# Kernel optimization log

Hardware: AMD Instinct MI355X
Metric: run time of the kernel (lower is better)

## Reference

```python
import jax, jax.numpy as jnp
import numpy as np

B, F, C, H, W = 16, 256, 64, 64, 64   # batch, features, z_channels(e_dim), height, width
N_E = 512                              # codebooksize
BETA = 1.0
EPS = 1e-5


def setup_inputs() -> dict:
    key = jax.random.key(0)
    ks = jax.random.split(key, 4)
    x = jax.random.normal(ks[0], (B, F, H, W), jnp.float32)
    emb = jax.random.normal(ks[1], (N_E, C), jnp.float32)
    emb = emb / jnp.linalg.norm(emb, axis=1, keepdims=True)  # points on hypersphere
    return dict(
        x=x,
        bn1_gamma=jnp.ones((F,), jnp.float32),
        bn1_beta=jnp.zeros((F,), jnp.float32),
        conv1_w=jax.random.normal(ks[2], (C, F), jnp.float32) * np.float32(1.0 / np.sqrt(F)),
        conv1_b=jnp.zeros((C,), jnp.float32),
        conv2_w=jax.random.normal(ks[3], (C, C), jnp.float32) * np.float32(1.0 / np.sqrt(C)),
        conv2_b=jnp.zeros((C,), jnp.float32),
        embedding=emb,
        r=jnp.ones((N_E,), jnp.float32),
    )


def reference(x, bn1_gamma, bn1_beta, conv1_w, conv1_b, conv2_w, conv2_b, embedding, r):
    sg = jax.lax.stop_gradient
    # BatchNorm2d (training mode: batch stats, biased variance)
    mu = x.mean(axis=(0, 2, 3), keepdims=True)
    var = x.var(axis=(0, 2, 3), keepdims=True)
    x1 = (x - mu) * jax.lax.rsqrt(var + EPS)
    x1 = x1 * bn1_gamma[None, :, None, None] + bn1_beta[None, :, None, None]
    # 1x1 convs (note: original overwrites norm2 output, conv2 consumes conv1 output directly)
    x1 = jnp.einsum('bfhw,cf->bchw', x1, conv1_w) + conv1_b[None, :, None, None]
    z = jnp.einsum('bchw,oc->bohw', x1, conv2_w) + conv2_b[None, :, None, None]

    zf = z.reshape(-1, C)  # [B*C*H*W/e_dim view == flat rows of e_dim]
    # codebook angular statistics (norms detached, as torch.Tensor(list) detaches)
    d1 = embedding @ embedding.T                                 # [n_e, n_e]
    en = sg(jnp.linalg.norm(embedding, axis=1))                  # [n_e]
    edx = jnp.clip(d1 / (en[:, None] * en[None, :]), -0.99999, 0.99999)
    ang = jnp.arccos(edx)
    total_min_distance = jnp.mean(jnp.sort(ang, axis=0)[1])      # kthvalue(.,2,dim=0)
    codebookvariance = jnp.mean(jnp.var(ang, axis=1, ddof=1))    # torch.var unbiased

    # VQ dispatch: squared L2 distances + argmin + gather
    d = (zf ** 2).sum(1, keepdims=True) + (embedding ** 2).sum(1) - 2.0 * (zf @ embedding.T)
    idx = jnp.argmin(d, axis=1)                                  # [ntok]
    z_q = embedding[idx].reshape(z.shape)

    hsw = jnp.mean(jnp.square(r - en))
    # legacy=True path with beta=1.0, ignorezq=False, disentangle=True
    loss = jnp.mean((sg(z_q) - z) ** 2) + BETA * jnp.mean((z_q - sg(z)) ** 2)
    loss = loss + hsw + (codebookvariance - total_min_distance)

    z_q = z + sg(z_q - z)  # straight-through
    cb_loss = jnp.float32(0.0)  # prev_cb is None
    r_c = r + sg(jnp.clip(r, 0.9, 1.1) - r)  # Clamp with straight-through grad
    mean_r = jnp.mean(r_c)
    return (loss, z_q, codebookvariance, total_min_distance, hsw, cb_loss, mean_r)
```

## Files before the change

### kernel.cpp

```cpp
#include <hip/hip_runtime.h>
#include <math.h>


#define CAP    2048
#define MARGIN 4e-3f

#define WS_WHI  0
#define WS_WLO  8192
#define WS_BP   16384
#define WS_EN   16448
#define WS_E2   16960
#define WS_ACC  17472
#define WS_CNT  17480
#define WS_WL   17488
#define WS_EFT  19536
#define WS_WD   52304
#define WS_BPD  85072
#define WS_PART 85200
#define WS_EHI  87248
#define WS_ELO  103632

typedef __attribute__((ext_vector_type(8))) __bf16 bf16v8;
typedef __attribute__((ext_vector_type(2))) __bf16 bf16v2;
typedef __attribute__((ext_vector_type(4))) float  f32v4;
typedef __attribute__((ext_vector_type(4))) unsigned u32v4;

__device__ __forceinline__ unsigned short f2bf(float f) {
    __bf16 h = (__bf16)f;
    return __builtin_bit_cast(unsigned short, h);
}
__device__ __forceinline__ float bf2f(unsigned short h) {
    union { unsigned u; float f; } v; v.u = ((unsigned)h) << 16; return v.f;
}
__device__ __forceinline__ unsigned pack_bf2(float a, float b) {
    bf16v2 v = { (__bf16)a, (__bf16)b };
    return __builtin_bit_cast(unsigned, v);
}
__device__ __forceinline__ float bfhi(float a) {
    return (float)(__bf16)a;
}
__device__ __forceinline__ void load_lds16(const float* g, unsigned* l) {
    __builtin_amdgcn_global_load_lds((const __attribute__((address_space(1))) void*)g,
                                     (__attribute__((address_space(3))) void*)l, 16, 0, 0);
}

__global__ __launch_bounds__(256) void bn_partial(
    const float* __restrict__ x, double* __restrict__ part)
{
    const int f = blockIdx.x >> 1, ch = blockIdx.x & 1, t = threadIdx.x;
    double s = 0.0, q = 0.0;
    #pragma unroll 1
    for (int bb = 0; bb < 8; ++bb) {
        const int b = ch * 8 + bb;
        const float4* p = (const float4*)(x + ((size_t)(b * 256 + f) << 12));
        #pragma unroll
        for (int ii = 0; ii < 4; ++ii) {
            float4 u = p[t + ii * 256];
            double dx = u.x, dy = u.y, dz = u.z, dw = u.w;
            s += (dx + dy) + (dz + dw);
            q = fma(dx, dx, q); q = fma(dy, dy, q);
            q = fma(dz, dz, q); q = fma(dw, dw, q);
        }
    }
    #pragma unroll
    for (int off = 32; off; off >>= 1) { s += __shfl_xor(s, off, 64); q += __shfl_xor(q, off, 64); }
    __shared__ double sh[8];
    const int wv = t >> 6;
    if ((t & 63) == 0) { sh[wv * 2] = s; sh[wv * 2 + 1] = q; }
    __syncthreads();
    if (t == 0) {
        part[blockIdx.x * 2]     = (sh[0] + sh[2]) + (sh[4] + sh[6]);
        part[blockIdx.x * 2 + 1] = (sh[1] + sh[3]) + (sh[5] + sh[7]);
    }
}

__global__ __launch_bounds__(256) void prep(
    const float* __restrict__ w1, const float* __restrict__ w2,
    const float* __restrict__ b1, const float* __restrict__ b2,
    const float* __restrict__ gamma, const float* __restrict__ beta,
    const float* __restrict__ emb, const double* __restrict__ part,
    unsigned short* __restrict__ whi, unsigned short* __restrict__ wlo,
    double* __restrict__ Wd,
    double* __restrict__ bpd, float* __restrict__ bp,
    float* __restrict__ eft, float* __restrict__ en, float* __restrict__ e2,
    unsigned short* __restrict__ ehi, unsigned short* __restrict__ elo,
    float* __restrict__ accs, int* __restrict__ cnt)
{
    __shared__ double sh_ad[4];
    __shared__ double cdl[256];
    __shared__ double red[4][64];
    __shared__ double tsh[64];
    const int t = threadIdx.x;

    if (blockIdx.x < 64) {
        const int o = t & 63, fi = t >> 6;
        const int f = blockIdx.x * 4 + fi;
        if (o == 0) {
            double s = part[(2 * f) * 2]     + part[(2 * f + 1) * 2];
            double q = part[(2 * f) * 2 + 1] + part[(2 * f + 1) * 2 + 1];
            double mean = s * (1.0 / 65536.0);
            double var  = q * (1.0 / 65536.0) - mean * mean;
            sh_ad[fi] = (double)gamma[f] / sqrt(var + 1e-5);
        }
        __syncthreads();
        double s = 0.0;
        for (int c = 0; c < 64; ++c)
            s = fma((double)w2[o * 64 + c], (double)w1[c * 256 + f], s);
        double wp = s * sh_ad[fi];
        Wd[o * 256 + f] = wp;
        {
            float wpf = (float)wp;
            unsigned short wh = f2bf(wpf);
            unsigned short wlv = f2bf(wpf - bf2f(wh));
            int mt = o >> 4, cq_ = o & 15, sK = f >> 5, qd_ = (f >> 3) & 3, j = f & 7;
            int idx = ((mt * 8 + sK) * 64 + qd_ * 16 + cq_) * 8 + j;
            whi[idx] = wh; wlo[idx] = wlv;
        }

        const int lane = t & 63, wv = t >> 6;
        #pragma unroll
        for (int rr = 0; rr < 2; ++rr) {
            int n = blockIdx.x * 8 + rr * 4 + wv;
            float v = emb[n * 64 + lane];
            eft[lane * 512 + n] = v;
            unsigned short hb = f2bf(v);
            unsigned short lb = f2bf(v - bf2f(hb));
            int pos = (lane >> 3) ^ (n & 7);
            ehi[n * 64 + pos * 8 + (lane & 7)] = hb;
            elo[n * 64 + pos * 8 + (lane & 7)] = lb;
            float qq = v * v;
            #pragma unroll
            for (int off = 32; off; off >>= 1) qq += __shfl_xor(qq, off, 64);
            if (lane == 0) { e2[n] = qq; en[n] = sqrtf(qq); }
        }
    } else {
        {
            const int f = t;
            double s = part[(2 * f) * 2]     + part[(2 * f + 1) * 2];
            double q = part[(2 * f) * 2 + 1] + part[(2 * f + 1) * 2 + 1];
            double mean = s * (1.0 / 65536.0);
            double var  = q * (1.0 / 65536.0) - mean * mean;
            double a = (double)gamma[f] / sqrt(var + 1e-5);
            cdl[f] = (double)beta[f] - mean * a;
        }
        __syncthreads();
        const int o = t & 63, p = t >> 6;
        double ss = 0.0;
        for (int j = 0; j < 64; ++j) {
            int fidx = p * 64 + j;
            ss = fma((double)w1[o * 256 + fidx], cdl[fidx], ss);
        }
        red[p][o] = ss; __syncthreads();
        if (t < 64) tsh[t] = (double)b1[t] + (red[0][t] + red[1][t]) + (red[2][t] + red[3][t]);
        __syncthreads();
        if (t < 64) {
            double bb = (double)b2[t];
            for (int c = 0; c < 64; ++c)
                bb = fma((double)w2[t * 64 + c], tsh[c], bb);
            bpd[t] = bb;
            bp[t]  = (float)bb;
        }
        if (t < 8) accs[t] = 0.f;
        if (t == 0) cnt[0] = 0;
    }
}

__global__ __launch_bounds__(256, 2) void fused_gemm_vq(
    const float* __restrict__ x,
    const unsigned short* __restrict__ whi,
    const unsigned short* __restrict__ wlo,
    const float* __restrict__ bp,
    const float* __restrict__ emb,
    const float* __restrict__ e2,
    const float* __restrict__ en,
    const float* __restrict__ eft,
    const unsigned short* __restrict__ ehi,
    const unsigned short* __restrict__ elo,
    float* __restrict__ accs,
    int* __restrict__ cnt, int* __restrict__ wl,
    float* __restrict__ zq)
{
    __shared__ __align__(16) unsigned smem[4880];
    enum { OAR = 0,
           OE2 = 4096, OZ2 = 4608, ODT = 4672, OD2T = 4736, OIT = 4800 };
    float* e2s = (float*)(smem + OE2);
    float* z2s = (float*)(smem + OZ2);
    float* dT  = (float*)(smem + ODT);
    float* d2T = (float*)(smem + OD2T);
    int*   iT  = (int*)(smem + OIT);

    const int tid = threadIdx.x, lane = tid & 63, wv = tid >> 6;

    if (blockIdx.x >= 1024) {
        const int i = blockIdx.x - 1024;
        float* ang = e2s;
        const float eni = en[i];
        const float* ei = emb + (i << 6);
        #pragma unroll
        for (int jj = 0; jj < 2; ++jj) {
            const int j = tid + jj * 256;
            float d0 = 0.f, d1 = 0.f, d2 = 0.f, d3 = 0.f;
            #pragma unroll
            for (int k = 0; k < 64; k += 4) {
                d0 = fmaf(ei[k + 0], eft[(k + 0) * 512 + j], d0);
                d1 = fmaf(ei[k + 1], eft[(k + 1) * 512 + j], d1);
                d2 = fmaf(ei[k + 2], eft[(k + 2) * 512 + j], d2);
                d3 = fmaf(ei[k + 3], eft[(k + 3) * 512 + j], d3);
            }
            float dot = (d0 + d1) + (d2 + d3);
            float xv = dot / (eni * en[j]);
            xv = fminf(fmaxf(xv, -0.99999f), 0.99999f);
            ang[j] = acosf(xv);
        }
        __syncthreads();
        if (wv == 0) {
            float m1 = 3.4e38f, m2 = 3.4e38f, ssum = 0.f;
            #pragma unroll
            for (int t8 = 0; t8 < 8; ++t8) {
                float a = ang[t8 * 64 + lane];
                ssum += a;
                if (a < m1) { m2 = m1; m1 = a; }
                else if (a < m2) m2 = a;
            }
            #pragma unroll
            for (int off = 32; off; off >>= 1) ssum += __shfl_xor(ssum, off, 64);
            #pragma unroll
            for (int off = 32; off; off >>= 1) {
                float o1 = __shfl_xor(m1, off, 64);
                float o2 = __shfl_xor(m2, off, 64);
                if (o1 < m1) { m2 = fminf(m1, o2); m1 = o1; }
                else          m2 = fminf(m2, o1);
            }
            float mean = ssum * (1.f / 512.f);
            float vs = 0.f;
            #pragma unroll
            for (int t8 = 0; t8 < 8; ++t8) {
                float tt = ang[t8 * 64 + lane] - mean;
                vs = fmaf(tt, tt, vs);
            }
            #pragma unroll
            for (int off = 32; off; off >>= 1) vs += __shfl_xor(vs, off, 64);
            if (lane == 0) {
                atomicAdd(accs + 1, vs * (1.f / 511.f));
                atomicAdd(accs + 2, m2);
            }
        }
        return;
    }

    const int wvu = __builtin_amdgcn_readfirstlane(wv);
    const int b = blockIdx.x >> 6, h = blockIdx.x & 63;
    const int cq = lane & 15, qd = lane >> 4;

    bf16v8 Ahi[8], Alo[8];
    #pragma unroll
    for (int s = 0; s < 8; ++s) {
        Ahi[s] = *(const bf16v8*)(whi + ((size_t)((wvu * 8 + s) * 64 + lane)) * 8);
        Alo[s] = *(const bf16v8*)(wlo + ((size_t)((wvu * 8 + s) * 64 + lane)) * 8);
    }
    float bpv[4];
    #pragma unroll
    for (int r = 0; r < 4; ++r) bpv[r] = bp[wvu * 16 + qd * 4 + r];
    e2s[tid]       = e2[tid];
    e2s[tid + 256] = e2[tid + 256];

    const float* xb = x + ((size_t)(b * 256 + wvu * 16) << 12) + (h << 6) + lane;
    float xv[16];
    #pragma unroll
    for (int i = 0; i < 16; ++i) xv[i] = xb[(size_t)i << 12];

    f32v4 acc[4];
    #pragma unroll
    for (int nt = 0; nt < 4; ++nt) acc[nt] = (f32v4){bpv[0], bpv[1], bpv[2], bpv[3]};

    #pragma unroll
    for (int chk = 0; chk < 4; ++chk) {
        __syncthreads();
        {
            unsigned hb[8], lb[8];
            #pragma unroll
            for (int p = 0; p < 8; ++p) {
                float a = xv[2 * p], bq = xv[2 * p + 1];
                hb[p] = pack_bf2(a, bq);
                lb[p] = pack_bf2(a - bfhi(a), bq - bfhi(bq));
            }
            const int b0 = lane * 32 + (((2 * wvu) ^ (lane & 7)) << 2);
            const int b1 = lane * 32 + (((2 * wvu + 1) ^ (lane & 7)) << 2);
            *(u32v4*)(smem + OAR + b0)        = (u32v4){hb[0], hb[1], hb[2], hb[3]};
            *(u32v4*)(smem + OAR + b1)        = (u32v4){hb[4], hb[5], hb[6], hb[7]};
            *(u32v4*)(smem + OAR + 2048 + b0) = (u32v4){lb[0], lb[1], lb[2], lb[3]};
            *(u32v4*)(smem + OAR + 2048 + b1) = (u32v4){lb[4], lb[5], lb[6], lb[7]};
        }
        __syncthreads();
        if (chk < 3) {
            const float* xb2 = xb + ((size_t)((chk + 1) * 64) << 12);
            #pragma unroll
            for (int i = 0; i < 16; ++i) xv[i] = xb2[(size_t)i << 12];
        }
        #pragma unroll
        for (int st2 = 0; st2 < 2; ++st2) {
            const int s = chk * 2 + st2;
            #pragma unroll
            for (int nt = 0; nt < 4; ++nt) {
                const int row = nt * 16 + cq;
                const int pos = row * 32 + (((st2 * 4 + qd) ^ (row & 7)) << 2);
                bf16v8 bh = *(const bf16v8*)(smem + OAR + pos);
                bf16v8 bl = *(const bf16v8*)(smem + OAR + 2048 + pos);
                acc[nt] = __builtin_amdgcn_mfma_f32_16x16x32_bf16(Ahi[s], bh, acc[nt], 0, 0, 0);
                acc[nt] = __builtin_amdgcn_mfma_f32_16x16x32_bf16(Ahi[s], bl, acc[nt], 0, 0, 0);
                acc[nt] = __builtin_amdgcn_mfma_f32_16x16x32_bf16(Alo[s], bh, acc[nt], 0, 0, 0);
            }
        }
    }
    __syncthreads();

    {
        float z2p[4];
        #pragma unroll
        for (int r = 0; r < 4; ++r) {
            float p2 = 0.f;
            #pragma unroll
            for (int nt = 0; nt < 4; ++nt) p2 = fmaf(acc[nt][r], acc[nt][r], p2);
            #pragma unroll
            for (int off = 1; off <= 8; off <<= 1) p2 += __shfl_xor(p2, off, 64);
            z2p[r] = p2;
        }
        if (cq == 0) {
            #pragma unroll
            for (int r = 0; r < 4; ++r) z2s[wvu * 16 + qd * 4 + r] = z2p[r];
        }
        unsigned short* ar = (unsigned short*)(smem + OAR);
        #pragma unroll
        for (int nt = 0; nt < 4; ++nt) {
            const int w = nt * 16 + cq;
            const int gz = w >> 3, kj = w & 7;
            #pragma unroll
            for (int r = 0; r < 4; ++r) {
                const int tok = wvu * 16 + qd * 4 + r;
                const int hw = tok * 64 + ((gz ^ (tok & 7)) << 3) + kj;
                unsigned short zh = f2bf(acc[nt][r]);
                ar[hw]        = zh;
                ar[4096 + hw] = f2bf(acc[nt][r] - bf2f(zh));
            }
        }
    }
    __syncthreads();

    const int x7 = cq & 7;
    bf16v8 vahi[2], valo[2];
    {
        const int rbase = (wvu * 16 + cq) * 32;
        #pragma unroll
        for (int s = 0; s < 2; ++s) {
            int pos = ((s * 4 + qd) ^ x7) * 4;
            vahi[s] = *(const bf16v8*)(smem + OAR + rbase + pos);
            valo[s] = *(const bf16v8*)(smem + OAR + 2048 + rbase + pos);
        }
    }
    __syncthreads();

    {
        const float* gh = (const float*)ehi;
        const float* gl = (const float*)elo;
        load_lds16(gh + wvu * 256 + lane * 4,        smem + OAR + wvu * 256);
        load_lds16(gl + wvu * 256 + lane * 4,        smem + OAR + 1024 + wvu * 256);
        load_lds16(gh + 1024 + wvu * 256 + lane * 4, smem + OAR + 2048 + wvu * 256);
        load_lds16(gl + 1024 + wvu * 256 + lane * 4, smem + OAR + 3072 + wvu * 256);
    }

    float m1[4] = {-3.4e38f, -3.4e38f, -3.4e38f, -3.4e38f};
    float m2[4] = {-3.4e38f, -3.4e38f, -3.4e38f, -3.4e38f};
    int   i1[4] = {0, 0, 0, 0};
    const int p0 = (qd ^ x7) * 4, p1 = ((4 + qd) ^ x7) * 4;

    #pragma unroll 1
    for (int t2 = 0; t2 < 32; ++t2) {
        if ((t2 & 1) == 0) {
            __syncthreads();
            int st = t2 >> 1;
            if (st >= 1 && st < 15) {
                const float* gh = (const float*)ehi + (size_t)(st + 1) * 1024;
                const float* gl = (const float*)elo + (size_t)(st + 1) * 1024;
                unsigned* dst = smem + OAR + ((st + 1) & 1) * 2048;
                load_lds16(gh + wvu * 256 + lane * 4, dst + wvu * 256);
                load_lds16(gl + wvu * 256 + lane * 4, dst + 1024 + wvu * 256);
            }
        }
        const int rb = OAR + ((t2 >> 1) & 1) * 2048 + ((t2 & 1) * 16 + cq) * 32;
        bf16v8 bh0 = *(const bf16v8*)(smem + rb + p0);
        bf16v8 bh1 = *(const bf16v8*)(smem + rb + p1);
        bf16v8 bl0 = *(const bf16v8*)(smem + rb + 1024 + p0);
        bf16v8 bl1 = *(const bf16v8*)(smem + rb + 1024 + p1);
        const float eps = e2s[t2 * 16 + cq];
        f32v4 a = {0.f, 0.f, 0.f, 0.f};
        __builtin_amdgcn_s_setprio(1);
        a = __builtin_amdgcn_mfma_f32_16x16x32_bf16(vahi[0], bh0, a, 0, 0, 0);
        a = __builtin_amdgcn_mfma_f32_16x16x32_bf16(vahi[1], bh1, a, 0, 0, 0);
        a = __builtin_amdgcn_mfma_f32_16x16x32_bf16(vahi[0], bl0, a, 0, 0, 0);
        a = __builtin_amdgcn_mfma_f32_16x16x32_bf16(vahi[1], bl1, a, 0, 0, 0);
        a = __builtin_amdgcn_mfma_f32_16x16x32_bf16(valo[0], bh0, a, 0, 0, 0);
        a = __builtin_amdgcn_mfma_f32_16x16x32_bf16(valo[1], bh1, a, 0, 0, 0);
        __builtin_amdgcn_s_setprio(0);
        const int n = t2 * 16 + cq;
        #pragma unroll
        for (int r = 0; r < 4; ++r) {
            float s = fmaf(-0.5f, eps, a[r]);
            bool gt = s > m1[r];
            m2[r] = fminf(fmaxf(s, m2[r]), m1[r]);
            i1[r] = gt ? n : i1[r];
            m1[r] = fmaxf(s, m1[r]);
        }
    }

    #pragma unroll
    for (int r = 0; r < 4; ++r) {
        #pragma unroll
        for (int off = 1; off <= 8; off <<= 1) {
            float o1 = __shfl_xor(m1[r], off, 64);
            float o2 = __shfl_xor(m2[r], off, 64);
            int   oi = __shfl_xor(i1[r], off, 64);
            if (o1 > m1[r] || (o1 == m1[r] && oi < i1[r])) {
                m2[r] = fmaxf(m1[r], o2); m1[r] = o1; i1[r] = oi;
            } else {
                m2[r] = fmaxf(m2[r], o1);
            }
        }
    }
    if (cq == 0) {
        #pragma unroll
        for (int r = 0; r < 4; ++r) {
            int tok = wvu * 16 + qd * 4 + r;
            dT[tok] = m1[r]; d2T[tok] = m2[r]; iT[tok] = i1[r];
        }
    }
    __syncthreads();

    if (wv == 0) {
        float s1 = dT[lane], s2 = d2T[lane];
        if (s1 - s2 < MARGIN * 0.5f) {
            int pos = atomicAdd(cnt, 1);
            if (pos < CAP) wl[pos] = ((b << 6) + lane) * 64 + h;
        }
        float ms = z2s[lane] - 2.f * s1;
        #pragma unroll
        for (int off = 32; off; off >>= 1) ms += __shfl_xor(ms, off, 64);
        if (lane == 0) atomicAdd(accs + 0, ms);
    }
    __syncthreads();

    float* zrow = zq + ((size_t)(b * 64) << 12) + (h << 6) + lane;
    #pragma unroll
    for (int cc = 0; cc < 16; ++cc) {
        int c = wvu * 16 + cc;
        int id = iT[c];
        zrow[(size_t)c << 12] = emb[(id << 6) + lane];
    }
}

__global__ __launch_bounds__(256) void refine_fin(
    const float* __restrict__ x,
    const double* __restrict__ Wd,
    const double* __restrict__ bpd,
    const float* __restrict__ emb,
    const float* __restrict__ eft,
    const int* __restrict__ cnt, const int* __restrict__ wl,
    float* __restrict__ zq,
    const float* __restrict__ accs, const float* __restrict__ en,
    const float* __restrict__ r, float* __restrict__ out)
{
    const int tid = threadIdx.x, lane = tid & 63, wv = tid >> 6;

    if (blockIdx.x == 256) {
        if (wv == 0) {
            float hs = 0.f, rs = 0.f;
            #pragma unroll
            for (int jj = 0; jj < 8; ++jj) {
                int n = (jj << 6) + lane;
                float rv = r[n];
                float d = rv - en[n];
                hs = fmaf(d, d, hs);
                rs += fminf(fmaxf(rv, 0.9f), 1.1f);
            }
            #pragma unroll
            for (int off = 32; off; off >>= 1) { hs += __shfl_xor(hs, off, 64); rs += __shfl_xor(rs, off, 64); }
            if (lane == 0) {
                float hsw    = hs * (1.f / 512.f);
                float mean_r = rs * (1.f / 512.f);
                float mse    = accs[0] * (1.f / 4194304.f);
                float cbv    = accs[1] * (1.f / 512.f);
                float tmd    = accs[2] * (1.f / 512.f);
                float loss   = 2.f * mse + hsw + (cbv - tmd);
                out[0]       = loss;
                out[4194305] = cbv;
                out[4194306] = tmd;
                out[4194307] = hsw;
                out[4194308] = 0.f;
                out[4194309] = mean_r;
            }
        }
        return;
    }

    int count = cnt[0]; if (count > CAP) count = CAP;

    __shared__ double zp[4][64];
    __shared__ double zs[64];
    __shared__ double dsh[256];
    __shared__ int    ish[256];

    for (int it = blockIdx.x; it < count; it += 256) {
        const int r2 = wl[it];
        const int b = r2 >> 12, c = (r2 >> 6) & 63, h = r2 & 63;

        const float* xp = x + (((size_t)(b * 256 + wv * 64)) << 12) + (h << 6) + lane;
        const double* wrow = Wd + c * 256 + wv * 64;
        double z0 = 0.0, z1 = 0.0, z2a = 0.0, z3 = 0.0;
        #pragma unroll
        for (int f = 0; f < 64; f += 4) {
            float a0 = xp[(size_t)(f + 0) << 12];
            float a1 = xp[(size_t)(f + 1) << 12];
            float a2 = xp[(size_t)(f + 2) << 12];
            float a3 = xp[(size_t)(f + 3) << 12];
            z0  = fma(wrow[f + 0], (double)a0, z0);
            z1  = fma(wrow[f + 1], (double)a1, z1);
            z2a = fma(wrow[f + 2], (double)a2, z2a);
            z3  = fma(wrow[f + 3], (double)a3, z3);
        }
        zp[wv][lane] = (z0 + z1) + (z2a + z3);
        __syncthreads();
        if (tid < 64) zs[tid] = (zp[0][tid] + zp[1][tid]) + (zp[2][tid] + zp[3][tid]) + bpd[c];
        __syncthreads();

        double dm = 1e300; int im = 0;
        #pragma unroll
        for (int jj = 0; jj < 2; ++jj) {
            int n = (jj << 8) + tid;
            double da = 0.0, db = 0.0;
            #pragma unroll 8
            for (int k = 0; k < 64; k += 2) {
                double t0 = zs[k]     - (double)eft[(k << 9) + n];
                double t1 = zs[k + 1] - (double)eft[((k + 1) << 9) + n];
                da = fma(t0, t0, da); db = fma(t1, t1, db);
            }
            double d = da + db;
            if (d < dm) { dm = d; im = n; }
        }
        dsh[tid] = dm; ish[tid] = im;
        __syncthreads();
        for (int st = 128; st; st >>= 1) {
            if (tid < st) {
                double od = dsh[tid + st]; int oi = ish[tid + st];
                if (od < dsh[tid] || (od == dsh[tid] && oi < ish[tid])) { dsh[tid] = od; ish[tid] = oi; }
            }
            __syncthreads();
        }
        if (tid < 64) {
            int idx = ish[0];
            zq[((size_t)r2 << 6) + tid] = emb[(idx << 6) + tid];
        }
        __syncthreads();
    }
}

extern "C" void kernel_launch(void* const* d_in, const int* in_sizes, int n_in,
                              void* d_out, int out_size, void* d_ws, size_t ws_size,
                              hipStream_t stream) {
    const float* x   = (const float*)d_in[0];
    const float* g1  = (const float*)d_in[1];
    const float* be1 = (const float*)d_in[2];
    const float* w1  = (const float*)d_in[3];
    const float* b1  = (const float*)d_in[4];
    const float* w2  = (const float*)d_in[5];
    const float* b2  = (const float*)d_in[6];
    const float* emb = (const float*)d_in[7];
    const float* r   = (const float*)d_in[8];
    float* ws = (float*)d_ws;
    float* out = (float*)d_out;

    double* WD   = (double*)(ws + WS_WD);
    double* BPD  = (double*)(ws + WS_BPD);
    double* PART = (double*)(ws + WS_PART);
    int*    CNT  = (int*)(ws + WS_CNT);
    int*    WL   = (int*)(ws + WS_WL);
    unsigned short* WHI = (unsigned short*)(ws + WS_WHI);
    unsigned short* WLO = (unsigned short*)(ws + WS_WLO);
    unsigned short* EHI = (unsigned short*)(ws + WS_EHI);
    unsigned short* ELO = (unsigned short*)(ws + WS_ELO);

    bn_partial<<<512, 256, 0, stream>>>(x, PART);
    prep<<<65, 256, 0, stream>>>(w1, w2, b1, b2, g1, be1, emb, PART,
                                 WHI, WLO, WD, BPD, ws + WS_BP,
                                 ws + WS_EFT, ws + WS_EN, ws + WS_E2,
                                 EHI, ELO, ws + WS_ACC, CNT);
    fused_gemm_vq<<<1536, 256, 0, stream>>>(x, WHI, WLO, ws + WS_BP,
                                            emb, ws + WS_E2, ws + WS_EN, ws + WS_EFT,
                                            EHI, ELO, ws + WS_ACC, CNT, WL, out + 1);
    refine_fin<<<257, 256, 0, stream>>>(x, WD, BPD, emb, ws + WS_EFT, CNT, WL,
                                        out + 1, ws + WS_ACC, ws + WS_EN, r, out);
}
```

Before: 185.9 us.

## Move codebook angle stats into BN stats kernel and split BN reduction finer

The 512 codebook-angle blocks move out of the fused GEMM/VQ kernel into the BN statistics kernel, computing norms directly from the embedding so they no longer depend on prep. This lets them overlap with the memory-bound BN pass and shrinks the GEMM grid to 1024 blocks. The BN partials are now split four ways per feature instead of two, giving more parallelism. Accumulator zeroing moves to a memset. The MFMA chain is also split into two independent accumulators and the refine distance loop gets four partial sums for more ILP. The codebook-stats blocks are recomputed from raw embeddings, which costs some extra arithmetic.

```diff
diff --git a/kernel.cpp b/kernel.cpp
--- a/kernel.cpp
+++ b/kernel.cpp
@@ -16,9 +16,9 @@
 #define WS_EFT  19536
 #define WS_WD   52304
 #define WS_BPD  85072
-#define WS_PART 85200
-#define WS_EHI  87248
-#define WS_ELO  103632
+#define WS_EHI  85200
+#define WS_ELO  101584
+#define WS_PART 117968
 
 typedef __attribute__((ext_vector_type(8))) __bf16 bf16v8;
 typedef __attribute__((ext_vector_type(2))) __bf16 bf16v2;
@@ -44,33 +44,109 @@
                                      (__attribute__((address_space(3))) void*)l, 16, 0, 0);
 }
 
-__global__ __launch_bounds__(256) void bn_partial(
-    const float* __restrict__ x, double* __restrict__ part)
+__global__ __launch_bounds__(256) void bn_stats(
+    const float* __restrict__ x, double* __restrict__ part,
+    const float* __restrict__ emb, float* __restrict__ accs)
 {
-    const int f = blockIdx.x >> 1, ch = blockIdx.x & 1, t = threadIdx.x;
-    double s = 0.0, q = 0.0;
-    #pragma unroll 1
-    for (int bb = 0; bb < 8; ++bb) {
-        const int b = ch * 8 + bb;
-        const float4* p = (const float4*)(x + ((size_t)(b * 256 + f) << 12));
-        #pragma unroll
-        for (int ii = 0; ii < 4; ++ii) {
-            float4 u = p[t + ii * 256];
-            double dx = u.x, dy = u.y, dz = u.z, dw = u.w;
-            s += (dx + dy) + (dz + dw);
-            q = fma(dx, dx, q); q = fma(dy, dy, q);
-            q = fma(dz, dz, q); q = fma(dw, dw, q);
-        }
-    }
-    #pragma unroll
-    for (int off = 32; off; off >>= 1) { s += __shfl_xor(s, off, 64); q += __shfl_xor(q, off, 64); }
-    __shared__ double sh[8];
-    const int wv = t >> 6;
-    if ((t & 63) == 0) { sh[wv * 2] = s; sh[wv * 2 + 1] = q; }
-    __syncthreads();
-    if (t == 0) {
-        part[blockIdx.x * 2]     = (sh[0] + sh[2]) + (sh[4] + sh[6]);
-        part[blockIdx.x * 2 + 1] = (sh[1] + sh[3]) + (sh[5] + sh[7]);
+    const int t = threadIdx.x;
+
+    if (blockIdx.x < 1024) {
+        const int f = blockIdx.x >> 2, ch = blockIdx.x & 3;
+        double s0 = 0.0, s1 = 0.0, q0 = 0.0, q1 = 0.0, q2 = 0.0, q3 = 0.0;
+        #pragma unroll
+        for (int bb = 0; bb < 4; ++bb) {
+            const int b = ch * 4 + bb;
+            const float4* p = (const float4*)(x + ((size_t)(b * 256 + f) << 12));
+            #pragma unroll
+            for (int ii = 0; ii < 4; ++ii) {
+                float4 u = p[t + ii * 256];
+                double dx = u.x, dy = u.y, dz = u.z, dw = u.w;
+                s0 += dx + dy; s1 += dz + dw;
+                q0 = fma(dx, dx, q0); q1 = fma(dy, dy, q1);
+                q2 = fma(dz, dz, q2); q3 = fma(dw, dw, q3);
+            }
+        }
+        double s = s0 + s1, q = (q0 + q1) + (q2 + q3);
+        #pragma unroll
+        for (int off = 32; off; off >>= 1) { s += __shfl_xor(s, off, 64); q += __shfl_xor(q, off, 64); }
+        __shared__ double sh[8];
+        const int wv = t >> 6;
+        if ((t & 63) == 0) { sh[wv * 2] = s; sh[wv * 2 + 1] = q; }
+        __syncthreads();
+        if (t == 0) {
+            part[blockIdx.x * 2]     = (sh[0] + sh[2]) + (sh[4] + sh[6]);
+            part[blockIdx.x * 2 + 1] = (sh[1] + sh[3]) + (sh[5] + sh[7]);
+        }
+    } else {
+        const int i = blockIdx.x - 1024;
+        const int lane = t & 63, wv = t >> 6;
+        __shared__ float ei_sh[64];
+        __shared__ float ang[512];
+        if (t < 64) ei_sh[t] = emb[(i << 6) + t];
+        __syncthreads();
+        float ni0 = 0.f, ni1 = 0.f, ni2 = 0.f, ni3 = 0.f;
+        #pragma unroll
+        for (int k = 0; k < 64; k += 4) {
+            ni0 = fmaf(ei_sh[k + 0], ei_sh[k + 0], ni0);
+            ni1 = fmaf(ei_sh[k + 1], ei_sh[k + 1], ni1);
+            ni2 = fmaf(ei_sh[k + 2], ei_sh[k + 2], ni2);
+            ni3 = fmaf(ei_sh[k + 3], ei_sh[k + 3], ni3);
+        }
+        const float eni = sqrtf((ni0 + ni1) + (ni2 + ni3));
+        #pragma unroll
+        for (int jj = 0; jj < 2; ++jj) {
+            const int j = t + jj * 256;
+            const float4* er = (const float4*)(emb + ((size_t)j << 6));
+            float d0 = 0.f, d1 = 0.f, d2 = 0.f, d3 = 0.f;
+            float n0 = 0.f, n1 = 0.f, n2 = 0.f, n3 = 0.f;
+            #pragma unroll
+            for (int k4 = 0; k4 < 16; ++k4) {
+                float4 u = er[k4];
+                const float* e4 = ei_sh + k4 * 4;
+                d0 = fmaf(u.x, e4[0], d0); d1 = fmaf(u.y, e4[1], d1);
+                d2 = fmaf(u.z, e4[2], d2); d3 = fmaf(u.w, e4[3], d3);
+                n0 = fmaf(u.x, u.x, n0);   n1 = fmaf(u.y, u.y, n1);
+                n2 = fmaf(u.z, u.z, n2);   n3 = fmaf(u.w, u.w, n3);
+            }
+            float dot = (d0 + d1) + (d2 + d3);
+            float enj = sqrtf((n0 + n1) + (n2 + n3));
+            float xv = dot / (eni * enj);
+            xv = fminf(fmaxf(xv, -0.99999f), 0.99999f);
+            ang[j] = acosf(xv);
+        }
+        __syncthreads();
+        if (wv == 0) {
+            float m1 = 3.4e38f, m2 = 3.4e38f, ssum = 0.f;
+            #pragma unroll
+            for (int t8 = 0; t8 < 8; ++t8) {
+                float a = ang[t8 * 64 + lane];
+                ssum += a;
+                if (a < m1) { m2 = m1; m1 = a; }
+                else if (a < m2) m2 = a;
+            }
+            #pragma unroll
+            for (int off = 32; off; off >>= 1) ssum += __shfl_xor(ssum, off, 64);
+            #pragma unroll
+            for (int off = 32; off; off >>= 1) {
+                float o1 = __shfl_xor(m1, off, 64);
+                float o2 = __shfl_xor(m2, off, 64);
+                if (o1 < m1) { m2 = fminf(m1, o2); m1 = o1; }
+                else          m2 = fminf(m2, o1);
+            }
+            float mean = ssum * (1.f / 512.f);
+            float vs = 0.f;
+            #pragma unroll
+            for (int t8 = 0; t8 < 8; ++t8) {
+                float tt = ang[t8 * 64 + lane] - mean;
+                vs = fmaf(tt, tt, vs);
+            }
+            #pragma unroll
+            for (int off = 32; off; off >>= 1) vs += __shfl_xor(vs, off, 64);
+            if (lane == 0) {
+                atomicAdd(accs + 1, vs * (1.f / 511.f));
+                atomicAdd(accs + 2, m2);
+            }
+        }
     }
 }
 
@@ -83,8 +159,7 @@
     double* __restrict__ Wd,
     double* __restrict__ bpd, float* __restrict__ bp,
     float* __restrict__ eft, float* __restrict__ en, float* __restrict__ e2,
-    unsigned short* __restrict__ ehi, unsigned short* __restrict__ elo,
-    float* __restrict__ accs, int* __restrict__ cnt)
+    unsigned short* __restrict__ ehi, unsigned short* __restrict__ elo)
 {
     __shared__ double sh_ad[4];
     __shared__ double cdl[256];
@@ -96,8 +171,10 @@
         const int o = t & 63, fi = t >> 6;
         const int f = blockIdx.x * 4 + fi;
         if (o == 0) {
-            double s = part[(2 * f) * 2]     + part[(2 * f + 1) * 2];
-            double q = part[(2 * f) * 2 + 1] + part[(2 * f + 1) * 2 + 1];
+            double s = (part[(4 * f) * 2]     + part[(4 * f + 1) * 2])
+                     + (part[(4 * f + 2) * 2] + part[(4 * f + 3) * 2]);
+            double q = (part[(4 * f) * 2 + 1]     + part[(4 * f + 1) * 2 + 1])
+                     + (part[(4 * f + 2) * 2 + 1] + part[(4 * f + 3) * 2 + 1]);
             double mean = s * (1.0 / 65536.0);
             double var  = q * (1.0 / 65536.0) - mean * mean;
             sh_ad[fi] = (double)gamma[f] / sqrt(var + 1e-5);
@@ -136,8 +213,10 @@
     } else {
         {
             const int f = t;
-            double s = part[(2 * f) * 2]     + part[(2 * f + 1) * 2];
-            double q = part[(2 * f) * 2 + 1] + part[(2 * f + 1) * 2 + 1];
+            double s = (part[(4 * f) * 2]     + part[(4 * f + 1) * 2])
+                     + (part[(4 * f + 2) * 2] + part[(4 * f + 3) * 2]);
+            double q = (part[(4 * f) * 2 + 1]     + part[(4 * f + 1) * 2 + 1])
+                     + (part[(4 * f + 2) * 2 + 1] + part[(4 * f + 3) * 2 + 1]);
             double mean = s * (1.0 / 65536.0);
             double var  = q * (1.0 / 65536.0) - mean * mean;
             double a = (double)gamma[f] / sqrt(var + 1e-5);
@@ -160,8 +239,6 @@
             bpd[t] = bb;
             bp[t]  = (float)bb;
         }
-        if (t < 8) accs[t] = 0.f;
-        if (t == 0) cnt[0] = 0;
     }
 }
 
@@ -172,8 +249,6 @@
     const float* __restrict__ bp,
     const float* __restrict__ emb,
     const float* __restrict__ e2,
-    const float* __restrict__ en,
-    const float* __restrict__ eft,
     const unsigned short* __restrict__ ehi,
     const unsigned short* __restrict__ elo,
     float* __restrict__ accs,
@@ -190,64 +265,6 @@
     int*   iT  = (int*)(smem + OIT);
 
     const int tid = threadIdx.x, lane = tid & 63, wv = tid >> 6;
-
-    if (blockIdx.x >= 1024) {
-        const int i = blockIdx.x - 1024;
-        float* ang = e2s;
-        const float eni = en[i];
-        const float* ei = emb + (i << 6);
-        #pragma unroll
-        for (int jj = 0; jj < 2; ++jj) {
-            const int j = tid + jj * 256;
-            float d0 = 0.f, d1 = 0.f, d2 = 0.f, d3 = 0.f;
-            #pragma unroll
-            for (int k = 0; k < 64; k += 4) {
-                d0 = fmaf(ei[k + 0], eft[(k + 0) * 512 + j], d0);
-                d1 = fmaf(ei[k + 1], eft[(k + 1) * 512 + j], d1);
-                d2 = fmaf(ei[k + 2], eft[(k + 2) * 512 + j], d2);
-                d3 = fmaf(ei[k + 3], eft[(k + 3) * 512 + j], d3);
-            }
-            float dot = (d0 + d1) + (d2 + d3);
-            float xv = dot / (eni * en[j]);
-            xv = fminf(fmaxf(xv, -0.99999f), 0.99999f);
-            ang[j] = acosf(xv);
-        }
-        __syncthreads();
-        if (wv == 0) {
-            float m1 = 3.4e38f, m2 = 3.4e38f, ssum = 0.f;
-            #pragma unroll
-            for (int t8 = 0; t8 < 8; ++t8) {
-                float a = ang[t8 * 64 + lane];
-                ssum += a;
-                if (a < m1) { m2 = m1; m1 = a; }
-                else if (a < m2) m2 = a;
-            }
-            #pragma unroll
-            for (int off = 32; off; off >>= 1) ssum += __shfl_xor(ssum, off, 64);
-            #pragma unroll
-            for (int off = 32; off; off >>= 1) {
-                float o1 = __shfl_xor(m1, off, 64);
-                float o2 = __shfl_xor(m2, off, 64);
-                if (o1 < m1) { m2 = fminf(m1, o2); m1 = o1; }
-                else          m2 = fminf(m2, o1);
-            }
-            float mean = ssum * (1.f / 512.f);
-            float vs = 0.f;
-            #pragma unroll
-            for (int t8 = 0; t8 < 8; ++t8) {
-                float tt = ang[t8 * 64 + lane] - mean;
-                vs = fmaf(tt, tt, vs);
-            }
-            #pragma unroll
-            for (int off = 32; off; off >>= 1) vs += __shfl_xor(vs, off, 64);
-            if (lane == 0) {
-                atomicAdd(accs + 1, vs * (1.f / 511.f));
-                atomicAdd(accs + 2, m2);
-            }
-        }
-        return;
-    }
-
     const int wvu = __builtin_amdgcn_readfirstlane(wv);
     const int b = blockIdx.x >> 6, h = blockIdx.x & 63;
     const int cq = lane & 15, qd = lane >> 4;
@@ -392,19 +409,19 @@
         bf16v8 bl0 = *(const bf16v8*)(smem + rb + 1024 + p0);
         bf16v8 bl1 = *(const bf16v8*)(smem + rb + 1024 + p1);
         const float eps = e2s[t2 * 16 + cq];
-        f32v4 a = {0.f, 0.f, 0.f, 0.f};
+        f32v4 a0 = {0.f, 0.f, 0.f, 0.f}, a1 = {0.f, 0.f, 0.f, 0.f};
         __builtin_amdgcn_s_setprio(1);
-        a = __builtin_amdgcn_mfma_f32_16x16x32_bf16(vahi[0], bh0, a, 0, 0, 0);
-        a = __builtin_amdgcn_mfma_f32_16x16x32_bf16(vahi[1], bh1, a, 0, 0, 0);
-        a = __builtin_amdgcn_mfma_f32_16x16x32_bf16(vahi[0], bl0, a, 0, 0, 0);
-        a = __builtin_amdgcn_mfma_f32_16x16x32_bf16(vahi[1], bl1, a, 0, 0, 0);
-        a = __builtin_amdgcn_mfma_f32_16x16x32_bf16(valo[0], bh0, a, 0, 0, 0);
-        a = __builtin_amdgcn_mfma_f32_16x16x32_bf16(valo[1], bh1, a, 0, 0, 0);
+        a0 = __builtin_amdgcn_mfma_f32_16x16x32_bf16(vahi[0], bh0, a0, 0, 0, 0);
+        a1 = __builtin_amdgcn_mfma_f32_16x16x32_bf16(vahi[1], bh1, a1, 0, 0, 0);
+        a0 = __builtin_amdgcn_mfma_f32_16x16x32_bf16(vahi[0], bl0, a0, 0, 0, 0);
+        a1 = __builtin_amdgcn_mfma_f32_16x16x32_bf16(vahi[1], bl1, a1, 0, 0, 0);
+        a0 = __builtin_amdgcn_mfma_f32_16x16x32_bf16(valo[0], bh0, a0, 0, 0, 0);
+        a1 = __builtin_amdgcn_mfma_f32_16x16x32_bf16(valo[1], bh1, a1, 0, 0, 0);
         __builtin_amdgcn_s_setprio(0);
         const int n = t2 * 16 + cq;
         #pragma unroll
         for (int r = 0; r < 4; ++r) {
-            float s = fmaf(-0.5f, eps, a[r]);
+            float s = fmaf(-0.5f, eps, a0[r] + a1[r]);
             bool gt = s > m1[r];
             m2[r] = fminf(fmaxf(s, m2[r]), m1[r]);
             i1[r] = gt ? n : i1[r];
@@ -535,14 +552,17 @@
         #pragma unroll
         for (int jj = 0; jj < 2; ++jj) {
             int n = (jj << 8) + tid;
-            double da = 0.0, db = 0.0;
-            #pragma unroll 8
-            for (int k = 0; k < 64; k += 2) {
-                double t0 = zs[k]     - (double)eft[(k << 9) + n];
+            double da = 0.0, db = 0.0, dc = 0.0, dd = 0.0;
+            #pragma unroll 4
+            for (int k = 0; k < 64; k += 4) {
+                double t0 = zs[k]     - (double)eft[((k + 0) << 9) + n];
                 double t1 = zs[k + 1] - (double)eft[((k + 1) << 9) + n];
+                double t2 = zs[k + 2] - (double)eft[((k + 2) << 9) + n];
+                double t3 = zs[k + 3] - (double)eft[((k + 3) << 9) + n];
                 da = fma(t0, t0, da); db = fma(t1, t1, db);
-            }
-            double d = da + db;
+                dc = fma(t2, t2, dc); dd = fma(t3, t3, dd);
+            }
+            double d = (da + db) + (dc + dd);
             if (d < dm) { dm = d; im = n; }
         }
         dsh[tid] = dm; ish[tid] = im;
@@ -587,13 +607,15 @@
     unsigned short* EHI = (unsigned short*)(ws + WS_EHI);
     unsigned short* ELO = (unsigned short*)(ws + WS_ELO);
 
-    bn_partial<<<512, 256, 0, stream>>>(x, PART);
+    hipMemsetAsync(ws + WS_ACC, 0, 16 * sizeof(float), stream);
+
+    bn_stats<<<1536, 256, 0, stream>>>(x, PART, emb, ws + WS_ACC);
     prep<<<65, 256, 0, stream>>>(w1, w2, b1, b2, g1, be1, emb, PART,
                                  WHI, WLO, WD, BPD, ws + WS_BP,
                                  ws + WS_EFT, ws + WS_EN, ws + WS_E2,
-                                 EHI, ELO, ws + WS_ACC, CNT);
-    fused_gemm_vq<<<1536, 256, 0, stream>>>(x, WHI, WLO, ws + WS_BP,
-                                            emb, ws + WS_E2, ws + WS_EN, ws + WS_EFT,
+                                 EHI, ELO);
+    fused_gemm_vq<<<1024, 256, 0, stream>>>(x, WHI, WLO, ws + WS_BP,
+                                            emb, ws + WS_E2,
                                             EHI, ELO, ws + WS_ACC, CNT, WL, out + 1);
     refine_fin<<<257, 256, 0, stream>>>(x, WD, BPD, emb, ws + WS_EFT, CNT, WL,
                                         out + 1, ws + WS_ACC, ws + WS_EN, r, out);
```

After: 195.7 us. 5.3% more time.

## Widen BN partial grid and give each refine candidate its own block

Applied to the files above, without the earlier changes.

Splits the batch-norm partial reduction four ways per feature instead of two and doubles its grid, adding more independent accumulators so more memory traffic is in flight. The refine kernel now launches one block per candidate row, up to the cap, instead of 256 blocks looping over the work list. It replaces the shared-memory tree argmin with wave shuffles plus a small cross-wave step. The cost is many empty blocks when the candidate count is low, plus a workspace layout shift to fit the larger partial buffer.

```diff
diff --git a/kernel.cpp b/kernel.cpp
--- a/kernel.cpp
+++ b/kernel.cpp
@@ -16,9 +16,9 @@
 #define WS_EFT  19536
 #define WS_WD   52304
 #define WS_BPD  85072
-#define WS_PART 85200
-#define WS_EHI  87248
-#define WS_ELO  103632
+#define WS_EHI  85200
+#define WS_ELO  101584
+#define WS_PART 117968
 
 typedef __attribute__((ext_vector_type(8))) __bf16 bf16v8;
 typedef __attribute__((ext_vector_type(2))) __bf16 bf16v2;
@@ -47,21 +47,23 @@
 __global__ __launch_bounds__(256) void bn_partial(
     const float* __restrict__ x, double* __restrict__ part)
 {
-    const int f = blockIdx.x >> 1, ch = blockIdx.x & 1, t = threadIdx.x;
-    double s = 0.0, q = 0.0;
-    #pragma unroll 1
-    for (int bb = 0; bb < 8; ++bb) {
-        const int b = ch * 8 + bb;
+    const int t = threadIdx.x;
+    const int f = blockIdx.x >> 2, ch = blockIdx.x & 3;
+    double s0 = 0.0, s1 = 0.0, q0 = 0.0, q1 = 0.0, q2 = 0.0, q3 = 0.0;
+    #pragma unroll
+    for (int bb = 0; bb < 4; ++bb) {
+        const int b = ch * 4 + bb;
         const float4* p = (const float4*)(x + ((size_t)(b * 256 + f) << 12));
         #pragma unroll
         for (int ii = 0; ii < 4; ++ii) {
             float4 u = p[t + ii * 256];
             double dx = u.x, dy = u.y, dz = u.z, dw = u.w;
-            s += (dx + dy) + (dz + dw);
-            q = fma(dx, dx, q); q = fma(dy, dy, q);
-            q = fma(dz, dz, q); q = fma(dw, dw, q);
-        }
-    }
+            s0 += dx + dy; s1 += dz + dw;
+            q0 = fma(dx, dx, q0); q1 = fma(dy, dy, q1);
+            q2 = fma(dz, dz, q2); q3 = fma(dw, dw, q3);
+        }
+    }
+    double s = s0 + s1, q = (q0 + q1) + (q2 + q3);
     #pragma unroll
     for (int off = 32; off; off >>= 1) { s += __shfl_xor(s, off, 64); q += __shfl_xor(q, off, 64); }
     __shared__ double sh[8];
@@ -96,8 +98,10 @@
         const int o = t & 63, fi = t >> 6;
         const int f = blockIdx.x * 4 + fi;
         if (o == 0) {
-            double s = part[(2 * f) * 2]     + part[(2 * f + 1) * 2];
-            double q = part[(2 * f) * 2 + 1] + part[(2 * f + 1) * 2 + 1];
+            double s = (part[(4 * f) * 2]     + part[(4 * f + 1) * 2])
+                     + (part[(4 * f + 2) * 2] + part[(4 * f + 3) * 2]);
+            double q = (part[(4 * f) * 2 + 1]     + part[(4 * f + 1) * 2 + 1])
+                     + (part[(4 * f + 2) * 2 + 1] + part[(4 * f + 3) * 2 + 1]);
             double mean = s * (1.0 / 65536.0);
             double var  = q * (1.0 / 65536.0) - mean * mean;
             sh_ad[fi] = (double)gamma[f] / sqrt(var + 1e-5);
@@ -136,8 +140,10 @@
     } else {
         {
             const int f = t;
-            double s = part[(2 * f) * 2]     + part[(2 * f + 1) * 2];
-            double q = part[(2 * f) * 2 + 1] + part[(2 * f + 1) * 2 + 1];
+            double s = (part[(4 * f) * 2]     + part[(4 * f + 1) * 2])
+                     + (part[(4 * f + 2) * 2] + part[(4 * f + 3) * 2]);
+            double q = (part[(4 * f) * 2 + 1]     + part[(4 * f + 1) * 2 + 1])
+                     + (part[(4 * f + 2) * 2 + 1] + part[(4 * f + 3) * 2 + 1]);
             double mean = s * (1.0 / 65536.0);
             double var  = q * (1.0 / 65536.0) - mean * mean;
             double a = (double)gamma[f] / sqrt(var + 1e-5);
@@ -470,7 +476,7 @@
 {
     const int tid = threadIdx.x, lane = tid & 63, wv = tid >> 6;
 
-    if (blockIdx.x == 256) {
+    if (blockIdx.x == 2048) {
         if (wv == 0) {
             float hs = 0.f, rs = 0.f;
             #pragma unroll
@@ -502,63 +508,85 @@
     }
 
     int count = cnt[0]; if (count > CAP) count = CAP;
+    const int it = blockIdx.x;
+    if (it >= count) return;
 
     __shared__ double zp[4][64];
     __shared__ double zs[64];
-    __shared__ double dsh[256];
-    __shared__ int    ish[256];
-
-    for (int it = blockIdx.x; it < count; it += 256) {
-        const int r2 = wl[it];
-        const int b = r2 >> 12, c = (r2 >> 6) & 63, h = r2 & 63;
-
+    __shared__ double dsh[4];
+    __shared__ int    ish[4];
+
+    const int r2 = wl[it];
+    const int b = r2 >> 12, c = (r2 >> 6) & 63, h = r2 & 63;
+
+    {
         const float* xp = x + (((size_t)(b * 256 + wv * 64)) << 12) + (h << 6) + lane;
         const double* wrow = Wd + c * 256 + wv * 64;
-        double z0 = 0.0, z1 = 0.0, z2a = 0.0, z3 = 0.0;
-        #pragma unroll
-        for (int f = 0; f < 64; f += 4) {
+        double zc0 = 0.0, zc1 = 0.0, zc2 = 0.0, zc3 = 0.0;
+        double zc4 = 0.0, zc5 = 0.0, zc6 = 0.0, zc7 = 0.0;
+        #pragma unroll
+        for (int f = 0; f < 64; f += 8) {
             float a0 = xp[(size_t)(f + 0) << 12];
             float a1 = xp[(size_t)(f + 1) << 12];
             float a2 = xp[(size_t)(f + 2) << 12];
             float a3 = xp[(size_t)(f + 3) << 12];
-            z0  = fma(wrow[f + 0], (double)a0, z0);
-            z1  = fma(wrow[f + 1], (double)a1, z1);
-            z2a = fma(wrow[f + 2], (double)a2, z2a);
-            z3  = fma(wrow[f + 3], (double)a3, z3);
-        }
-        zp[wv][lane] = (z0 + z1) + (z2a + z3);
-        __syncthreads();
-        if (tid < 64) zs[tid] = (zp[0][tid] + zp[1][tid]) + (zp[2][tid] + zp[3][tid]) + bpd[c];
-        __syncthreads();
-
-        double dm = 1e300; int im = 0;
-        #pragma unroll
-        for (int jj = 0; jj < 2; ++jj) {
-            int n = (jj << 8) + tid;
-            double da = 0.0, db = 0.0;
-            #pragma unroll 8
-            for (int k = 0; k < 64; k += 2) {
-                double t0 = zs[k]     - (double)eft[(k << 9) + n];
-                double t1 = zs[k + 1] - (double)eft[((k + 1) << 9) + n];
-                da = fma(t0, t0, da); db = fma(t1, t1, db);
-            }
-            double d = da + db;
-            if (d < dm) { dm = d; im = n; }
-        }
-        dsh[tid] = dm; ish[tid] = im;
-        __syncthreads();
-        for (int st = 128; st; st >>= 1) {
-            if (tid < st) {
-                double od = dsh[tid + st]; int oi = ish[tid + st];
-                if (od < dsh[tid] || (od == dsh[tid] && oi < ish[tid])) { dsh[tid] = od; ish[tid] = oi; }
-            }
-            __syncthreads();
-        }
-        if (tid < 64) {
-            int idx = ish[0];
-            zq[((size_t)r2 << 6) + tid] = emb[(idx << 6) + tid];
-        }
-        __syncthreads();
+            float a4 = xp[(size_t)(f + 4) << 12];
+            float a5 = xp[(size_t)(f + 5) << 12];
+            float a6 = xp[(size_t)(f + 6) << 12];
+            float a7 = xp[(size_t)(f + 7) << 12];
+            zc0 = fma(wrow[f + 0], (double)a0, zc0);
+            zc1 = fma(wrow[f + 1], (double)a1, zc1);
+            zc2 = fma(wrow[f + 2], (double)a2, zc2);
+            zc3 = fma(wrow[f + 3], (double)a3, zc3);
+            zc4 = fma(wrow[f + 4], (double)a4, zc4);
+            zc5 = fma(wrow[f + 5], (double)a5, zc5);
+            zc6 = fma(wrow[f + 6], (double)a6, zc6);
+            zc7 = fma(wrow[f + 7], (double)a7, zc7);
+        }
+        zp[wv][lane] = ((zc0 + zc1) + (zc2 + zc3)) + ((zc4 + zc5) + (zc6 + zc7));
+    }
+    __syncthreads();
+    if (tid < 64) zs[tid] = (zp[0][tid] + zp[1][tid]) + (zp[2][tid] + zp[3][tid]) + bpd[c];
+    __syncthreads();
+
+    const int n0 = tid, n1 = tid + 256;
+    double d0a = 0.0, d0b = 0.0, d0c = 0.0, d0d = 0.0;
+    double d1a = 0.0, d1b = 0.0, d1c = 0.0, d1d = 0.0;
+    #pragma unroll 4
+    for (int k = 0; k < 64; k += 4) {
+        double z0 = zs[k], z1 = zs[k + 1], z2 = zs[k + 2], z3 = zs[k + 3];
+        double t;
+        t = z0 - (double)eft[((k + 0) << 9) + n0]; d0a = fma(t, t, d0a);
+        t = z1 - (double)eft[((k + 1) << 9) + n0]; d0b = fma(t, t, d0b);
+        t = z2 - (double)eft[((k + 2) << 9) + n0]; d0c = fma(t, t, d0c);
+        t = z3 - (double)eft[((k + 3) << 9) + n0]; d0d = fma(t, t, d0d);
+        t = z0 - (double)eft[((k + 0) << 9) + n1]; d1a = fma(t, t, d1a);
+        t = z1 - (double)eft[((k + 1) << 9) + n1]; d1b = fma(t, t, d1b);
+        t = z2 - (double)eft[((k + 2) << 9) + n1]; d1c = fma(t, t, d1c);
+        t = z3 - (double)eft[((k + 3) << 9) + n1]; d1d = fma(t, t, d1d);
+    }
+    double d0 = (d0a + d0b) + (d0c + d0d);
+    double d1 = (d1a + d1b) + (d1c + d1d);
+    double dm; int im;
+    if (d1 < d0) { dm = d1; im = n1; } else { dm = d0; im = n0; }
+
+    #pragma unroll
+    for (int off = 32; off; off >>= 1) {
+        double od = __shfl_xor(dm, off, 64);
+        int    oi = __shfl_xor(im, off, 64);
+        if (od < dm || (od == dm && oi < im)) { dm = od; im = oi; }
+    }
+    if (lane == 0) { dsh[wv] = dm; ish[wv] = im; }
+    __syncthreads();
+
+    if (tid < 64) {
+        double best = dsh[0]; int bi = ish[0];
+        #pragma unroll
+        for (int wq = 1; wq < 4; ++wq) {
+            double od = dsh[wq]; int oi = ish[wq];
+            if (od < best || (od == best && oi < bi)) { best = od; bi = oi; }
+        }
+        zq[((size_t)r2 << 6) + tid] = emb[(bi << 6) + tid];
     }
 }
 
@@ -587,7 +615,7 @@
     unsigned short* EHI = (unsigned short*)(ws + WS_EHI);
     unsigned short* ELO = (unsigned short*)(ws + WS_ELO);
 
-    bn_partial<<<512, 256, 0, stream>>>(x, PART);
+    bn_partial<<<1024, 256, 0, stream>>>(x, PART);
     prep<<<65, 256, 0, stream>>>(w1, w2, b1, b2, g1, be1, emb, PART,
                                  WHI, WLO, WD, BPD, ws + WS_BP,
                                  ws + WS_EFT, ws + WS_EN, ws + WS_E2,
@@ -595,6 +623,6 @@
     fused_gemm_vq<<<1536, 256, 0, stream>>>(x, WHI, WLO, ws + WS_BP,
                                             emb, ws + WS_E2, ws + WS_EN, ws + WS_EFT,
                                             EHI, ELO, ws + WS_ACC, CNT, WL, out + 1);
-    refine_fin<<<257, 256, 0, stream>>>(x, WD, BPD, emb, ws + WS_EFT, CNT, WL,
-                                        out + 1, ws + WS_ACC, ws + WS_EN, r, out);
-}
+    refine_fin<<<2049, 256, 0, stream>>>(x, WD, BPD, emb, ws + WS_EFT, CNT, WL,
+                                         out + 1, ws + WS_ACC, ws + WS_EN, r, out);
+}
```

Result: no change. 182.9 us (-1.6%).
